# Kernel tuning notes

Measured on AMD Instinct MI355X. Metric: run time of the kernel, lower is better.

The kernel has to match this reference:

```python
import jax, jax.numpy as jnp
import numpy as np

N = 50000      # num_nodes
R = 8          # num_relations
H = 128        # hidden_channels
C = 40         # num_classes
E = 800000     # num_edges


def _seg_mean_over_relations(msgs, dst, etype):
    """Per-relation mean aggregation (PyG RGCNConv aggr='mean'), summed over relations.
    msgs: [E, H] per-edge messages; dst: [E] target nodes; etype: [E] relation ids.
    Returns [N, H].
    """
    seg = dst * R + etype                                   # [E] combined (node, relation) id
    sums = jax.ops.segment_sum(msgs, seg, num_segments=N * R)          # [N*R, H]
    cnt = jax.ops.segment_sum(jnp.ones((msgs.shape[0], 1), msgs.dtype), seg,
                              num_segments=N * R)                       # [N*R, 1]
    mean = sums / jnp.maximum(cnt, 1.0)
    return mean.reshape(N, R, -1).sum(axis=1)               # [N, H]


def setup_inputs() -> dict:
    key = jax.random.key(0)
    ks = jax.random.split(key, 10)
    s = 0.02
    edge_index = jax.random.randint(ks[0], (2, E), 0, N, dtype=jnp.int32)
    edge_type = jax.random.randint(ks[1], (E,), 0, R, dtype=jnp.int32)
    return {
        "edge_index": edge_index,
        "edge_type": edge_type,
        "W1": jax.random.normal(ks[2], (R, N, H), jnp.float32) * s,    # featureless: embedding per (rel, node)
        "root1": jax.random.normal(ks[3], (N, H), jnp.float32) * s,    # root embedding (x=None)
        "b1": jnp.zeros((H,), jnp.float32),
        "W2": jax.random.normal(ks[4], (R, H, H), jnp.float32) * s,
        "root2": jax.random.normal(ks[5], (H, H), jnp.float32) * s,
        "b2": jnp.zeros((H,), jnp.float32),
        "lin_w": jax.random.normal(ks[6], (H, C), jnp.float32) * s,
        "lin_b": jnp.zeros((C,), jnp.float32),
    }


def reference(edge_index, edge_type, W1, root1, b1, W2, root2, b2, lin_w, lin_b):
    src, dst = edge_index[0], edge_index[1]  # flow: source_to_target

    # ---- layer 1 (featureless RGCNConv): gather relation-specific node embeddings ----
    msgs1 = W1[edge_type, src]                               # [E, H]
    h = _seg_mean_over_relations(msgs1, dst, edge_type)      # [N, H]
    h = h + root1 + b1
    h = jax.nn.relu(h)

    # ---- layer 2: relation-specific dense transform then gather-scatter ----
    xr = jnp.einsum('nh,rhk->rnk', h, W2)                    # [R, N, H]
    msgs2 = xr[edge_type, src]                               # [E, H]
    h2 = _seg_mean_over_relations(msgs2, dst, edge_type)     # [N, H]
    h2 = h2 + h @ root2 + b2
    h2 = jax.nn.relu(h2)

    # ---- final linear ----
    return h2 @ lin_w + lin_b                                # [N, C]
```

## Files before the change

kernel.cpp:

```cpp
#include <hip/hip_runtime.h>

#define HH 128
#define RNUM 8
#define CC 40
#define CAP 64
#define LDA 136
#define SRCMASK 0x7FFFFFF

typedef __attribute__((ext_vector_type(8))) short short8;
typedef __attribute__((ext_vector_type(4))) float floatx4;

__device__ __forceinline__ float u2f(unsigned u) {
    union { unsigned u; float f; } c;
    c.u = u;
    return c.f;
}
__device__ __forceinline__ unsigned short f2bf(float f) {
    union { float f; unsigned u; } c;
    c.f = f;
    return (unsigned short)((c.u + 0x7FFFu + ((c.u >> 16) & 1u)) >> 16);
}

__global__ void fill1_kernel(const int* __restrict__ src, const int* __restrict__ dst,
                             const int* __restrict__ et, int* __restrict__ deg,
                             int* __restrict__ elist, int E) {
    int e = blockIdx.x * blockDim.x + threadIdx.x;
    if (e < E) {
        int d = dst[e];
        int p = atomicAdd(&deg[d], 1);
        if (p < CAP) elist[(size_t)d * CAP + p] = (int)(((unsigned)et[e] << 27) | (unsigned)src[e]);
    }
}

__global__ void gather1_kernel(const int* __restrict__ deg, const int* __restrict__ elist,
                               const float* __restrict__ W1, const float* __restrict__ root1,
                               const float* __restrict__ b1, unsigned short* __restrict__ hbf,
                               int Nn) {
    int w = (blockIdx.x * blockDim.x + threadIdx.x) >> 6;
    if (w >= Nn) return;
    int lane = threadIdx.x & 63;
    int qid = lane >> 4, cl = lane & 15;
    int dd = min(deg[w], CAP);
    int pk = elist[(size_t)w * CAP + lane];
    int myrel = (lane < dd) ? (int)((unsigned)pk >> 27) : 8;

    float myinv = 1.0f;
#pragma unroll
    for (int r = 0; r < 8; ++r) {
        unsigned long long m = __ballot(myrel == r);
        int c = __popcll(m);
        if (lane == r) myinv = 1.0f / fmaxf(1.0f, (float)c);
    }

    float s0[8] = {0.f, 0.f, 0.f, 0.f, 0.f, 0.f, 0.f, 0.f};
    float s1[8] = {0.f, 0.f, 0.f, 0.f, 0.f, 0.f, 0.f, 0.f};
    float s2[8] = {0.f, 0.f, 0.f, 0.f, 0.f, 0.f, 0.f, 0.f};
    float s3[8] = {0.f, 0.f, 0.f, 0.f, 0.f, 0.f, 0.f, 0.f};

#define GRP(G, S)                                                                 \
    {                                                                             \
        int j = ((G) << 2) + qid;                                                 \
        int jj = min(j, dd - 1);                                                  \
        int pkj = __shfl(pk, jj);                                                 \
        int rr = (int)((unsigned)pkj >> 27);                                      \
        float wt = __shfl(myinv, rr);                                             \
        int ss = pkj & SRCMASK;                                                   \
        const float* p = W1 + ((size_t)rr * Nn + ss) * HH + cl * 8;               \
        if (j < dd) {                                                             \
            float4 v0 = *(const float4*)p;                                        \
            float4 v1 = *(const float4*)(p + 4);                                  \
            S[0] += v0.x * wt; S[1] += v0.y * wt; S[2] += v0.z * wt; S[3] += v0.w * wt; \
            S[4] += v1.x * wt; S[5] += v1.y * wt; S[6] += v1.z * wt; S[7] += v1.w * wt; \
        }                                                                         \
    }

    int ng = (dd + 3) >> 2;
    int g = 0;
    for (; g + 3 < ng; g += 4) {
        GRP(g, s0);
        GRP(g + 1, s1);
        GRP(g + 2, s2);
        GRP(g + 3, s3);
    }
    for (; g < ng; ++g) GRP(g, s0);
#undef GRP

#pragma unroll
    for (int k = 0; k < 8; ++k) {
        s0[k] += s1[k] + s2[k] + s3[k];
        s0[k] += __shfl_xor(s0[k], 16);
        s0[k] += __shfl_xor(s0[k], 32);
    }

    if (qid == 0) {
        const float* rp = root1 + (size_t)w * HH + cl * 8;
        float4 r0 = *(const float4*)rp;
        float4 r1 = *(const float4*)(rp + 4);
        float4 c0 = *(const float4*)(b1 + cl * 8);
        float4 c1 = *(const float4*)(b1 + cl * 8 + 4);
        float o[8];
        o[0] = fmaxf(s0[0] + r0.x + c0.x, 0.f); o[1] = fmaxf(s0[1] + r0.y + c0.y, 0.f);
        o[2] = fmaxf(s0[2] + r0.z + c0.z, 0.f); o[3] = fmaxf(s0[3] + r0.w + c0.w, 0.f);
        o[4] = fmaxf(s0[4] + r1.x + c1.x, 0.f); o[5] = fmaxf(s0[5] + r1.y + c1.y, 0.f);
        o[6] = fmaxf(s0[6] + r1.z + c1.z, 0.f); o[7] = fmaxf(s0[7] + r1.w + c1.w, 0.f);
        ushort4 pk0, pk1;
        pk0.x = f2bf(o[0]); pk0.y = f2bf(o[1]); pk0.z = f2bf(o[2]); pk0.w = f2bf(o[3]);
        pk1.x = f2bf(o[4]); pk1.y = f2bf(o[5]); pk1.z = f2bf(o[6]); pk1.w = f2bf(o[7]);
        unsigned short* hp = hbf + (size_t)w * HH + cl * 8;
        *(ushort4*)hp = pk0;
        *(ushort4*)(hp + 4) = pk1;
    }
}

__global__ void agg_kernel(const int* __restrict__ deg, const int* __restrict__ elist,
                           const unsigned short* __restrict__ hbf,
                           unsigned short* __restrict__ aggr, int Nn) {
    int w = (blockIdx.x * blockDim.x + threadIdx.x) >> 6;
    int d = w >> 1;
    if (d >= Nn) return;
    int half = w & 1;
    int lane = threadIdx.x & 63;
    int qid = lane >> 4, cl = lane & 15;
    int dd = min(deg[d], CAP);
    int pk = elist[(size_t)d * CAP + lane];
    int myrel = (lane < dd) ? (int)((unsigned)pk >> 27) : 8;

#define ACC8(V, S)                                                 \
    {                                                              \
        S[0] += u2f(V.x << 16); S[1] += u2f(V.x & 0xFFFF0000u);    \
        S[2] += u2f(V.y << 16); S[3] += u2f(V.y & 0xFFFF0000u);    \
        S[4] += u2f(V.z << 16); S[5] += u2f(V.z & 0xFFFF0000u);    \
        S[6] += u2f(V.w << 16); S[7] += u2f(V.w & 0xFFFF0000u);    \
    }

#pragma unroll
    for (int ri = 0; ri < 4; ++ri) {
        int r = half * 4 + ri;
        unsigned long long m = __ballot(myrel == r);
        int c = __popcll(m);
        float inv = 1.0f / fmaxf(1.0f, (float)c);
        float s[8] = {0.f, 0.f, 0.f, 0.f, 0.f, 0.f, 0.f, 0.f};
        int idx = 0;
        while (m) {
            int j = __ffsll((unsigned long long)m) - 1;
            m &= m - 1;
            int pkj = __shfl(pk, j);
            if ((idx & 3) == qid) {
                int ss = pkj & SRCMASK;
                uint4 v = *(const uint4*)(hbf + (size_t)ss * HH + cl * 8);
                ACC8(v, s);
            }
            ++idx;
        }
#pragma unroll
        for (int k = 0; k < 8; ++k) {
            s[k] += __shfl_xor(s[k], 16);
            s[k] += __shfl_xor(s[k], 32);
        }
        if (qid == 0) {
            ushort4 p0, p1;
            p0.x = f2bf(s[0] * inv); p0.y = f2bf(s[1] * inv);
            p0.z = f2bf(s[2] * inv); p0.w = f2bf(s[3] * inv);
            p1.x = f2bf(s[4] * inv); p1.y = f2bf(s[5] * inv);
            p1.z = f2bf(s[6] * inv); p1.w = f2bf(s[7] * inv);
            unsigned short* ap = aggr + ((size_t)d * RNUM + r) * HH + cl * 8;
            *(ushort4*)ap = p0;
            *(ushort4*)(ap + 4) = p1;
        }
    }
#undef ACC8
}

__global__ void tcast_kernel(const float* __restrict__ root2, const float* __restrict__ W2,
                             unsigned short* __restrict__ Bt) {
    int bid = blockIdx.x;
    int c = bid >> 5;
    int id = (bid & 31) * 256 + threadIdx.x;
    int n = id >> 6, kp = id & 63;
    const float* B = (c == 0) ? root2 : W2 + (size_t)(c - 1) * HH * HH;
    float f0 = B[(2 * kp) * HH + n];
    float f1 = B[(2 * kp + 1) * HH + n];
    unsigned v = (unsigned)f2bf(f0) | ((unsigned)f2bf(f1) << 16);
    *(unsigned*)(Bt + (size_t)c * HH * HH + n * HH + 2 * kp) = v;
}

__global__ __launch_bounds__(256, 3) void gemm9_kernel(
    const unsigned short* __restrict__ hbf, const unsigned short* __restrict__ aggr,
    const unsigned short* __restrict__ Bt, const float* __restrict__ b2,
    const float* __restrict__ lin_w, const float* __restrict__ lin_b,
    float* __restrict__ out, int Nn) {
    __shared__ unsigned short As[64 * LDA];
    __shared__ unsigned short Bs[128 * LDA];
    const int tid = threadIdx.x;
    const int lane = tid & 63, wv = tid >> 6;
    const int quad = lane >> 4, l16 = lane & 15;
    const int mr = wv & 1, nc = wv >> 1;
    const int m0 = blockIdx.x * 64;

    floatx4 acc[2][4];
#pragma unroll
    for (int a = 0; a < 2; ++a)
#pragma unroll
        for (int bb = 0; bb < 4; ++bb) acc[a][bb] = (floatx4){0.f, 0.f, 0.f, 0.f};

    for (int c = 0; c < 9; ++c) {
        __syncthreads();
        const unsigned short* Bsrc = Bt + (size_t)c * HH * HH;
#pragma unroll
        for (int it = 0; it < 8; ++it) {
            int id = tid + it * 256;
            int rw = id >> 4, c8 = id & 15;
            *(uint4*)(Bs + rw * LDA + c8 * 8) = *(const uint4*)(Bsrc + rw * HH + c8 * 8);
        }
#pragma unroll
        for (int it = 0; it < 4; ++it) {
            int id = tid + it * 256;
            int rw = id >> 4, c8 = id & 15;
            uint4 v = make_uint4(0, 0, 0, 0);
            if (m0 + rw < Nn) {
                const unsigned short* Asrc =
                    (c == 0) ? (hbf + (size_t)(m0 + rw) * HH)
                             : (aggr + ((size_t)(m0 + rw) * RNUM + (c - 1)) * HH);
                v = *(const uint4*)(Asrc + c8 * 8);
            }
            *(uint4*)(As + rw * LDA + c8 * 8) = v;
        }
        __syncthreads();
#pragma unroll
        for (int ks = 0; ks < 4; ++ks) {
            short8 a0 = *(const short8*)(As + (mr * 32 + l16) * LDA + ks * 32 + quad * 8);
            short8 a1 = *(const short8*)(As + (mr * 32 + 16 + l16) * LDA + ks * 32 + quad * 8);
#pragma unroll
            for (int nf = 0; nf < 4; ++nf) {
                short8 b = *(const short8*)(Bs + (nc * 64 + nf * 16 + l16) * LDA + ks * 32 + quad * 8);
                acc[0][nf] = __builtin_amdgcn_mfma_f32_16x16x32_bf16(a0, b, acc[0][nf], 0, 0, 0);
                acc[1][nf] = __builtin_amdgcn_mfma_f32_16x16x32_bf16(a1, b, acc[1][nf], 0, 0, 0);
            }
        }
    }

    __syncthreads();
#pragma unroll
    for (int mf = 0; mf < 2; ++mf)
#pragma unroll
        for (int nf = 0; nf < 4; ++nf) {
            int gcol = nc * 64 + nf * 16 + l16;
            float bb = b2[gcol];
#pragma unroll
            for (int rg = 0; rg < 4; ++rg) {
                int row = mr * 32 + mf * 16 + quad * 4 + rg;
                float v = fmaxf(acc[mf][nf][rg] + bb, 0.f);
                As[row * LDA + gcol] = f2bf(v);
            }
        }
    for (int it = 0; it < 20; ++it) {
        int id = tid + it * 256;
        int n = id >> 7, k = id & 127;
        Bs[n * LDA + k] = f2bf(lin_w[k * CC + n]);
    }
    __syncthreads();

    floatx4 acc2[3];
#pragma unroll
    for (int nf = 0; nf < 3; ++nf) acc2[nf] = (floatx4){0.f, 0.f, 0.f, 0.f};
#pragma unroll
    for (int ks = 0; ks < 4; ++ks) {
        short8 a = *(const short8*)(As + (wv * 16 + l16) * LDA + ks * 32 + quad * 8);
#pragma unroll
        for (int nf = 0; nf < 3; ++nf) {
            short8 b = *(const short8*)(Bs + (nf * 16 + l16) * LDA + ks * 32 + quad * 8);
            acc2[nf] = __builtin_amdgcn_mfma_f32_16x16x32_bf16(a, b, acc2[nf], 0, 0, 0);
        }
    }
#pragma unroll
    for (int nf = 0; nf < 3; ++nf) {
        int col = nf * 16 + l16;
        if (col < CC) {
            float lb = lin_b[col];
#pragma unroll
            for (int rg = 0; rg < 4; ++rg) {
                int grow = m0 + wv * 16 + quad * 4 + rg;
                if (grow < Nn) out[(size_t)grow * CC + col] = acc2[nf][rg] + lb;
            }
        }
    }
}


extern "C" void kernel_launch(void* const* d_in, const int* in_sizes, int n_in,
                              void* d_out, int out_size, void* d_ws, size_t ws_size,
                              hipStream_t stream) {
    const int* ei      = (const int*)d_in[0];
    const int* et      = (const int*)d_in[1];
    const float* W1    = (const float*)d_in[2];
    const float* root1 = (const float*)d_in[3];
    const float* b1    = (const float*)d_in[4];
    const float* W2    = (const float*)d_in[5];
    const float* root2 = (const float*)d_in[6];
    const float* b2    = (const float*)d_in[7];
    const float* lw    = (const float*)d_in[8];
    const float* lb    = (const float*)d_in[9];
    float* out = (float*)d_out;

    const int E = in_sizes[1];
    const int N = in_sizes[3] / HH;

    int* deg   = (int*)d_ws;
    int* elist = deg + N;
    size_t iofs = (size_t)N + (size_t)N * CAP;
    iofs = (iofs + 3) & ~(size_t)3;
    unsigned short* hbf  = (unsigned short*)((int*)d_ws + iofs);
    unsigned short* Bt   = hbf + (size_t)N * HH;
    unsigned short* aggr = Bt + (size_t)9 * HH * HH;

    const int* src = ei;
    const int* dst = ei + E;

    hipMemsetAsync(deg, 0, (size_t)N * sizeof(int), stream);
    fill1_kernel<<<(E + 255) / 256, 256, 0, stream>>>(src, dst, et, deg, elist, E);

    tcast_kernel<<<9 * 32, 256, 0, stream>>>(root2, W2, Bt);

    gather1_kernel<<<(N * 64 + 255) / 256, 256, 0, stream>>>(deg, elist, W1, root1, b1, hbf, N);
    agg_kernel<<<(N * 2 * 64 + 255) / 256, 256, 0, stream>>>(deg, elist, hbf, aggr, N);
    gemm9_kernel<<<(N + 63) / 64, 256, 0, stream>>>(hbf, aggr, Bt, b2, lw, lb, out, N);
}
```

Measured before the change: 538.2 us.

## Transform-then-gather for layer 2 and pad degree counters

Layer 2 now runs the dense per-relation transform first: a GEMM computes xr = h @ W2[r] (plus the root transform) for all nodes into a bf16 buffer. A second gather kernel then pulls transformed rows per edge, takes the per-relation mean and applies bias and ReLU, and a separate small kernel does the final linear layer. This replaces the previous aggregate-then-GEMM path, which wrote an N×8×128 per-relation aggregate and ran a 9-chunk GEMM. Degree counters are also spaced 16 ints apart to reduce atomic contention, at the cost of a larger memset and workspace, and it adds an extra kernel plus a 9×N×128 intermediate buffer.

Result: faster. 480.5 us (-10.7%).

```diff
diff --git a/kernel.cpp b/kernel.cpp
--- a/kernel.cpp
+++ b/kernel.cpp
@@ -6,6 +6,7 @@
 #define CAP 64
 #define LDA 136
 #define SRCMASK 0x7FFFFFF
+#define DEGSTR 16
 
 typedef __attribute__((ext_vector_type(8))) short short8;
 typedef __attribute__((ext_vector_type(4))) float floatx4;
@@ -21,15 +22,28 @@
     return (unsigned short)((c.u + 0x7FFFu + ((c.u >> 16) & 1u)) >> 16);
 }
 
-__global__ void fill1_kernel(const int* __restrict__ src, const int* __restrict__ dst,
-                             const int* __restrict__ et, int* __restrict__ deg,
-                             int* __restrict__ elist, int E) {
+__global__ void fill_kernel(const int* __restrict__ src, const int* __restrict__ dst,
+                            const int* __restrict__ et, int* __restrict__ deg,
+                            int* __restrict__ elist, int E) {
     int e = blockIdx.x * blockDim.x + threadIdx.x;
     if (e < E) {
         int d = dst[e];
-        int p = atomicAdd(&deg[d], 1);
+        int p = atomicAdd(&deg[(size_t)d * DEGSTR], 1);
         if (p < CAP) elist[(size_t)d * CAP + p] = (int)(((unsigned)et[e] << 27) | (unsigned)src[e]);
     }
+}
+
+__global__ void tcast_kernel(const float* __restrict__ root2, const float* __restrict__ W2,
+                             unsigned short* __restrict__ Bt) {
+    int bid = blockIdx.x;
+    int c = bid >> 5;
+    int id = (bid & 31) * 256 + threadIdx.x;
+    int n = id >> 6, kp = id & 63;
+    const float* B = (c == 0) ? root2 : W2 + (size_t)(c - 1) * HH * HH;
+    float g0 = B[(2 * kp) * HH + n];
+    float g1 = B[(2 * kp + 1) * HH + n];
+    unsigned v = (unsigned)f2bf(g0) | ((unsigned)f2bf(g1) << 16);
+    *(unsigned*)(Bt + (size_t)c * HH * HH + n * HH + 2 * kp) = v;
 }
 
 __global__ void gather1_kernel(const int* __restrict__ deg, const int* __restrict__ elist,
@@ -40,7 +54,7 @@
     if (w >= Nn) return;
     int lane = threadIdx.x & 63;
     int qid = lane >> 4, cl = lane & 15;
-    int dd = min(deg[w], CAP);
+    int dd = min(deg[(size_t)w * DEGSTR], CAP);
     int pk = elist[(size_t)w * CAP + lane];
     int myrel = (lane < dd) ? (int)((unsigned)pk >> 27) : 8;
 
@@ -112,90 +126,35 @@
     }
 }
 
-__global__ void agg_kernel(const int* __restrict__ deg, const int* __restrict__ elist,
-                           const unsigned short* __restrict__ hbf,
-                           unsigned short* __restrict__ aggr, int Nn) {
-    int w = (blockIdx.x * blockDim.x + threadIdx.x) >> 6;
-    int d = w >> 1;
-    if (d >= Nn) return;
-    int half = w & 1;
-    int lane = threadIdx.x & 63;
-    int qid = lane >> 4, cl = lane & 15;
-    int dd = min(deg[d], CAP);
-    int pk = elist[(size_t)d * CAP + lane];
-    int myrel = (lane < dd) ? (int)((unsigned)pk >> 27) : 8;
-
-#define ACC8(V, S)                                                 \
-    {                                                              \
-        S[0] += u2f(V.x << 16); S[1] += u2f(V.x & 0xFFFF0000u);    \
-        S[2] += u2f(V.y << 16); S[3] += u2f(V.y & 0xFFFF0000u);    \
-        S[4] += u2f(V.z << 16); S[5] += u2f(V.z & 0xFFFF0000u);    \
-        S[6] += u2f(V.w << 16); S[7] += u2f(V.w & 0xFFFF0000u);    \
-    }
-
-#pragma unroll
-    for (int ri = 0; ri < 4; ++ri) {
-        int r = half * 4 + ri;
-        unsigned long long m = __ballot(myrel == r);
-        int c = __popcll(m);
-        float inv = 1.0f / fmaxf(1.0f, (float)c);
-        float s[8] = {0.f, 0.f, 0.f, 0.f, 0.f, 0.f, 0.f, 0.f};
-        int idx = 0;
-        while (m) {
-            int j = __ffsll((unsigned long long)m) - 1;
-            m &= m - 1;
-            int pkj = __shfl(pk, j);
-            if ((idx & 3) == qid) {
-                int ss = pkj & SRCMASK;
-                uint4 v = *(const uint4*)(hbf + (size_t)ss * HH + cl * 8);
-                ACC8(v, s);
-            }
-            ++idx;
-        }
-#pragma unroll
-        for (int k = 0; k < 8; ++k) {
-            s[k] += __shfl_xor(s[k], 16);
-            s[k] += __shfl_xor(s[k], 32);
-        }
-        if (qid == 0) {
-            ushort4 p0, p1;
-            p0.x = f2bf(s[0] * inv); p0.y = f2bf(s[1] * inv);
-            p0.z = f2bf(s[2] * inv); p0.w = f2bf(s[3] * inv);
-            p1.x = f2bf(s[4] * inv); p1.y = f2bf(s[5] * inv);
-            p1.z = f2bf(s[6] * inv); p1.w = f2bf(s[7] * inv);
-            unsigned short* ap = aggr + ((size_t)d * RNUM + r) * HH + cl * 8;
-            *(ushort4*)ap = p0;
-            *(ushort4*)(ap + 4) = p1;
-        }
-    }
-#undef ACC8
-}
-
-__global__ void tcast_kernel(const float* __restrict__ root2, const float* __restrict__ W2,
-                             unsigned short* __restrict__ Bt) {
-    int bid = blockIdx.x;
-    int c = bid >> 5;
-    int id = (bid & 31) * 256 + threadIdx.x;
-    int n = id >> 6, kp = id & 63;
-    const float* B = (c == 0) ? root2 : W2 + (size_t)(c - 1) * HH * HH;
-    float f0 = B[(2 * kp) * HH + n];
-    float f1 = B[(2 * kp + 1) * HH + n];
-    unsigned v = (unsigned)f2bf(f0) | ((unsigned)f2bf(f1) << 16);
-    *(unsigned*)(Bt + (size_t)c * HH * HH + n * HH + 2 * kp) = v;
-}
-
-__global__ __launch_bounds__(256, 3) void gemm9_kernel(
-    const unsigned short* __restrict__ hbf, const unsigned short* __restrict__ aggr,
-    const unsigned short* __restrict__ Bt, const float* __restrict__ b2,
-    const float* __restrict__ lin_w, const float* __restrict__ lin_b,
-    float* __restrict__ out, int Nn) {
+__global__ __launch_bounds__(256, 3) void gemmxr_kernel(
+    const unsigned short* __restrict__ hbf, const unsigned short* __restrict__ Bt,
+    unsigned short* __restrict__ xrb, int Nn, int nmb) {
     __shared__ unsigned short As[64 * LDA];
     __shared__ unsigned short Bs[128 * LDA];
     const int tid = threadIdx.x;
     const int lane = tid & 63, wv = tid >> 6;
     const int quad = lane >> 4, l16 = lane & 15;
     const int mr = wv & 1, nc = wv >> 1;
-    const int m0 = blockIdx.x * 64;
+    const int mb = blockIdx.x % nmb;
+    const int c = blockIdx.x / nmb;
+    const int m0 = mb * 64;
+
+#pragma unroll
+    for (int it = 0; it < 4; ++it) {
+        int id = tid + it * 256;
+        int rw = id >> 4, c8 = id & 15;
+        uint4 v = make_uint4(0, 0, 0, 0);
+        if (m0 + rw < Nn) v = *(const uint4*)(hbf + (size_t)(m0 + rw) * HH + c8 * 8);
+        *(uint4*)(As + rw * LDA + c8 * 8) = v;
+    }
+    const unsigned short* Bsrc = Bt + (size_t)c * HH * HH;
+#pragma unroll
+    for (int it = 0; it < 8; ++it) {
+        int id = tid + it * 256;
+        int rw = id >> 4, c8 = id & 15;
+        *(uint4*)(Bs + rw * LDA + c8 * 8) = *(const uint4*)(Bsrc + rw * HH + c8 * 8);
+    }
+    __syncthreads();
 
     floatx4 acc[2][4];
 #pragma unroll
@@ -203,60 +162,146 @@
 #pragma unroll
         for (int bb = 0; bb < 4; ++bb) acc[a][bb] = (floatx4){0.f, 0.f, 0.f, 0.f};
 
-    for (int c = 0; c < 9; ++c) {
-        __syncthreads();
-        const unsigned short* Bsrc = Bt + (size_t)c * HH * HH;
-#pragma unroll
-        for (int it = 0; it < 8; ++it) {
-            int id = tid + it * 256;
-            int rw = id >> 4, c8 = id & 15;
-            *(uint4*)(Bs + rw * LDA + c8 * 8) = *(const uint4*)(Bsrc + rw * HH + c8 * 8);
+#pragma unroll
+    for (int ks = 0; ks < 4; ++ks) {
+        short8 a0 = *(const short8*)(As + (mr * 32 + l16) * LDA + ks * 32 + quad * 8);
+        short8 a1 = *(const short8*)(As + (mr * 32 + 16 + l16) * LDA + ks * 32 + quad * 8);
+#pragma unroll
+        for (int nf = 0; nf < 4; ++nf) {
+            short8 b = *(const short8*)(Bs + (nc * 64 + nf * 16 + l16) * LDA + ks * 32 + quad * 8);
+            acc[0][nf] = __builtin_amdgcn_mfma_f32_16x16x32_bf16(a0, b, acc[0][nf], 0, 0, 0);
+            acc[1][nf] = __builtin_amdgcn_mfma_f32_16x16x32_bf16(a1, b, acc[1][nf], 0, 0, 0);
         }
-#pragma unroll
-        for (int it = 0; it < 4; ++it) {
-            int id = tid + it * 256;
-            int rw = id >> 4, c8 = id & 15;
-            uint4 v = make_uint4(0, 0, 0, 0);
-            if (m0 + rw < Nn) {
-                const unsigned short* Asrc =
-                    (c == 0) ? (hbf + (size_t)(m0 + rw) * HH)
-                             : (aggr + ((size_t)(m0 + rw) * RNUM + (c - 1)) * HH);
-                v = *(const uint4*)(Asrc + c8 * 8);
-            }
-            *(uint4*)(As + rw * LDA + c8 * 8) = v;
-        }
-        __syncthreads();
-#pragma unroll
-        for (int ks = 0; ks < 4; ++ks) {
-            short8 a0 = *(const short8*)(As + (mr * 32 + l16) * LDA + ks * 32 + quad * 8);
-            short8 a1 = *(const short8*)(As + (mr * 32 + 16 + l16) * LDA + ks * 32 + quad * 8);
-#pragma unroll
-            for (int nf = 0; nf < 4; ++nf) {
-                short8 b = *(const short8*)(Bs + (nc * 64 + nf * 16 + l16) * LDA + ks * 32 + quad * 8);
-                acc[0][nf] = __builtin_amdgcn_mfma_f32_16x16x32_bf16(a0, b, acc[0][nf], 0, 0, 0);
-                acc[1][nf] = __builtin_amdgcn_mfma_f32_16x16x32_bf16(a1, b, acc[1][nf], 0, 0, 0);
+    }
+
+    __syncthreads();
+#pragma unroll
+    for (int mf = 0; mf < 2; ++mf)
+#pragma unroll
+        for (int nf = 0; nf < 4; ++nf) {
+            int gcol = nc * 64 + nf * 16 + l16;
+#pragma unroll
+            for (int rg = 0; rg < 4; ++rg) {
+                int row = mr * 32 + mf * 16 + quad * 4 + rg;
+                Bs[row * LDA + gcol] = f2bf(acc[mf][nf][rg]);
             }
         }
-    }
-
     __syncthreads();
 #pragma unroll
-    for (int mf = 0; mf < 2; ++mf)
-#pragma unroll
-        for (int nf = 0; nf < 4; ++nf) {
-            int gcol = nc * 64 + nf * 16 + l16;
-            float bb = b2[gcol];
-#pragma unroll
-            for (int rg = 0; rg < 4; ++rg) {
-                int row = mr * 32 + mf * 16 + quad * 4 + rg;
-                float v = fmaxf(acc[mf][nf][rg] + bb, 0.f);
-                As[row * LDA + gcol] = f2bf(v);
-            }
-        }
-    for (int it = 0; it < 20; ++it) {
+    for (int it = 0; it < 4; ++it) {
+        int id = tid + it * 256;
+        int rw = id >> 4, c8 = id & 15;
+        if (m0 + rw < Nn)
+            *(uint4*)(xrb + ((size_t)c * Nn + m0 + rw) * HH + c8 * 8) =
+                *(const uint4*)(Bs + rw * LDA + c8 * 8);
+    }
+}
+
+__global__ void gather2_kernel(const int* __restrict__ deg, const int* __restrict__ elist,
+                               const unsigned short* __restrict__ xrb, const float* __restrict__ b2,
+                               unsigned short* __restrict__ h2bf, int Nn) {
+    int w = (blockIdx.x * blockDim.x + threadIdx.x) >> 6;
+    if (w >= Nn) return;
+    int lane = threadIdx.x & 63;
+    int qid = lane >> 4, cl = lane & 15;
+    int dd = min(deg[(size_t)w * DEGSTR], CAP);
+    int pk = elist[(size_t)w * CAP + lane];
+    int myrel = (lane < dd) ? (int)((unsigned)pk >> 27) : 8;
+
+    float myinv = 1.0f;
+#pragma unroll
+    for (int r = 0; r < 8; ++r) {
+        unsigned long long m = __ballot(myrel == r);
+        int c = __popcll(m);
+        if (lane == r) myinv = 1.0f / fmaxf(1.0f, (float)c);
+    }
+
+    float s0[8] = {0.f, 0.f, 0.f, 0.f, 0.f, 0.f, 0.f, 0.f};
+    float s1[8] = {0.f, 0.f, 0.f, 0.f, 0.f, 0.f, 0.f, 0.f};
+    float s2[8] = {0.f, 0.f, 0.f, 0.f, 0.f, 0.f, 0.f, 0.f};
+    float s3[8] = {0.f, 0.f, 0.f, 0.f, 0.f, 0.f, 0.f, 0.f};
+
+#define GRP(G, S)                                                                 \
+    {                                                                             \
+        int j = ((G) << 2) + qid;                                                 \
+        int jj = min(j, dd - 1);                                                  \
+        int pkj = __shfl(pk, jj);                                                 \
+        int rr = (int)((unsigned)pkj >> 27);                                      \
+        float wt = __shfl(myinv, rr);                                             \
+        int ss = pkj & SRCMASK;                                                   \
+        const unsigned short* p = xrb + ((size_t)(rr + 1) * Nn + ss) * HH + cl * 8; \
+        if (j < dd) {                                                             \
+            uint4 v = *(const uint4*)p;                                           \
+            S[0] += u2f(v.x << 16) * wt; S[1] += u2f(v.x & 0xFFFF0000u) * wt;     \
+            S[2] += u2f(v.y << 16) * wt; S[3] += u2f(v.y & 0xFFFF0000u) * wt;     \
+            S[4] += u2f(v.z << 16) * wt; S[5] += u2f(v.z & 0xFFFF0000u) * wt;     \
+            S[6] += u2f(v.w << 16) * wt; S[7] += u2f(v.w & 0xFFFF0000u) * wt;     \
+        }                                                                         \
+    }
+
+    int ng = (dd + 3) >> 2;
+    int g = 0;
+    for (; g + 3 < ng; g += 4) {
+        GRP(g, s0);
+        GRP(g + 1, s1);
+        GRP(g + 2, s2);
+        GRP(g + 3, s3);
+    }
+    for (; g < ng; ++g) GRP(g, s0);
+#undef GRP
+
+#pragma unroll
+    for (int k = 0; k < 8; ++k) {
+        s0[k] += s1[k] + s2[k] + s3[k];
+        s0[k] += __shfl_xor(s0[k], 16);
+        s0[k] += __shfl_xor(s0[k], 32);
+    }
+
+    if (qid == 0) {
+        uint4 sv = *(const uint4*)(xrb + (size_t)w * HH + cl * 8);
+        float4 c0 = *(const float4*)(b2 + cl * 8);
+        float4 c1 = *(const float4*)(b2 + cl * 8 + 4);
+        float o[8];
+        o[0] = fmaxf(s0[0] + u2f(sv.x << 16) + c0.x, 0.f);
+        o[1] = fmaxf(s0[1] + u2f(sv.x & 0xFFFF0000u) + c0.y, 0.f);
+        o[2] = fmaxf(s0[2] + u2f(sv.y << 16) + c0.z, 0.f);
+        o[3] = fmaxf(s0[3] + u2f(sv.y & 0xFFFF0000u) + c0.w, 0.f);
+        o[4] = fmaxf(s0[4] + u2f(sv.z << 16) + c1.x, 0.f);
+        o[5] = fmaxf(s0[5] + u2f(sv.z & 0xFFFF0000u) + c1.y, 0.f);
+        o[6] = fmaxf(s0[6] + u2f(sv.w << 16) + c1.z, 0.f);
+        o[7] = fmaxf(s0[7] + u2f(sv.w & 0xFFFF0000u) + c1.w, 0.f);
+        ushort4 p0, p1;
+        p0.x = f2bf(o[0]); p0.y = f2bf(o[1]); p0.z = f2bf(o[2]); p0.w = f2bf(o[3]);
+        p1.x = f2bf(o[4]); p1.y = f2bf(o[5]); p1.z = f2bf(o[6]); p1.w = f2bf(o[7]);
+        unsigned short* hp = h2bf + (size_t)w * HH + cl * 8;
+        *(ushort4*)hp = p0;
+        *(ushort4*)(hp + 4) = p1;
+    }
+}
+
+__global__ __launch_bounds__(256, 4) void linout_kernel(
+    const unsigned short* __restrict__ h2, const float* __restrict__ lin_w,
+    const float* __restrict__ lin_b, float* __restrict__ out, int Nn) {
+    __shared__ unsigned short As[64 * LDA];
+    __shared__ unsigned short Bs[48 * LDA];
+    const int tid = threadIdx.x;
+    const int lane = tid & 63, wv = tid >> 6;
+    const int quad = lane >> 4, l16 = lane & 15;
+    const int m0 = blockIdx.x * 64;
+
+#pragma unroll
+    for (int it = 0; it < 4; ++it) {
+        int id = tid + it * 256;
+        int rw = id >> 4, c8 = id & 15;
+        uint4 v = make_uint4(0, 0, 0, 0);
+        if (m0 + rw < Nn) v = *(const uint4*)(h2 + (size_t)(m0 + rw) * HH + c8 * 8);
+        *(uint4*)(As + rw * LDA + c8 * 8) = v;
+    }
+#pragma unroll
+    for (int it = 0; it < 24; ++it) {
         int id = tid + it * 256;
         int n = id >> 7, k = id & 127;
-        Bs[n * LDA + k] = f2bf(lin_w[k * CC + n]);
+        Bs[n * LDA + k] = (n < CC) ? f2bf(lin_w[(size_t)k * CC + n]) : (unsigned short)0;
     }
     __syncthreads();
 
@@ -306,22 +351,24 @@
     const int N = in_sizes[3] / HH;
 
     int* deg   = (int*)d_ws;
-    int* elist = deg + N;
-    size_t iofs = (size_t)N + (size_t)N * CAP;
+    int* elist = deg + (size_t)N * DEGSTR;
+    size_t iofs = (size_t)N * DEGSTR + (size_t)N * CAP;
     iofs = (iofs + 3) & ~(size_t)3;
     unsigned short* hbf  = (unsigned short*)((int*)d_ws + iofs);
     unsigned short* Bt   = hbf + (size_t)N * HH;
-    unsigned short* aggr = Bt + (size_t)9 * HH * HH;
+    unsigned short* xrb  = Bt + (size_t)9 * HH * HH;
+    unsigned short* h2bf = xrb + (size_t)9 * N * HH;
 
     const int* src = ei;
     const int* dst = ei + E;
 
-    hipMemsetAsync(deg, 0, (size_t)N * sizeof(int), stream);
-    fill1_kernel<<<(E + 255) / 256, 256, 0, stream>>>(src, dst, et, deg, elist, E);
-
+    const int nmb = (N + 63) / 64;
+
+    hipMemsetAsync(deg, 0, (size_t)N * DEGSTR * sizeof(int), stream);
+    fill_kernel<<<(E + 255) / 256, 256, 0, stream>>>(src, dst, et, deg, elist, E);
     tcast_kernel<<<9 * 32, 256, 0, stream>>>(root2, W2, Bt);
-
     gather1_kernel<<<(N * 64 + 255) / 256, 256, 0, stream>>>(deg, elist, W1, root1, b1, hbf, N);
-    agg_kernel<<<(N * 2 * 64 + 255) / 256, 256, 0, stream>>>(deg, elist, hbf, aggr, N);
-    gemm9_kernel<<<(N + 63) / 64, 256, 0, stream>>>(hbf, aggr, Bt, b2, lw, lb, out, N);
-}
+    gemmxr_kernel<<<nmb * 9, 256, 0, stream>>>(hbf, Bt, xrb, N, nmb);
+    gather2_kernel<<<(N * 64 + 255) / 256, 256, 0, stream>>>(deg, elist, xrb, b2, h2bf, N);
+    linout_kernel<<<nmb, 256, 0, stream>>>(h2bf, lw, lb, out, N);
+}
```

## Fuse layer-2 aggregation into the GEMM kernel and pad degree counters

Applied to the files above, without the earlier changes.

Merges the per-relation mean aggregation into the layer-2 GEMM kernel. Each block gathers neighbor rows for 32 nodes straight into shared memory, so the [N,8,128] aggr buffer is never written to or read back from global memory. B tiles are now read directly from global memory instead of being staged in LDS, and occupancy drops to 2 blocks per SM because of the larger shared tile. Degree counters are spread 16 ints apart, apparently to reduce atomic contention in the fill kernel, at the cost of a larger memset.

After: 580.0 us. 7.8% more time.

```diff
diff --git a/kernel.cpp b/kernel.cpp
--- a/kernel.cpp
+++ b/kernel.cpp
@@ -6,6 +6,7 @@
 #define CAP 64
 #define LDA 136
 #define SRCMASK 0x7FFFFFF
+#define DEGSTR 16
 
 typedef __attribute__((ext_vector_type(8))) short short8;
 typedef __attribute__((ext_vector_type(4))) float floatx4;
@@ -21,15 +22,28 @@
     return (unsigned short)((c.u + 0x7FFFu + ((c.u >> 16) & 1u)) >> 16);
 }
 
-__global__ void fill1_kernel(const int* __restrict__ src, const int* __restrict__ dst,
-                             const int* __restrict__ et, int* __restrict__ deg,
-                             int* __restrict__ elist, int E) {
+__global__ void fill_kernel(const int* __restrict__ src, const int* __restrict__ dst,
+                            const int* __restrict__ et, int* __restrict__ deg,
+                            int* __restrict__ elist, int E) {
     int e = blockIdx.x * blockDim.x + threadIdx.x;
     if (e < E) {
         int d = dst[e];
-        int p = atomicAdd(&deg[d], 1);
+        int p = atomicAdd(&deg[(size_t)d * DEGSTR], 1);
         if (p < CAP) elist[(size_t)d * CAP + p] = (int)(((unsigned)et[e] << 27) | (unsigned)src[e]);
     }
+}
+
+__global__ void tcast_kernel(const float* __restrict__ root2, const float* __restrict__ W2,
+                             unsigned short* __restrict__ Bt) {
+    int bid = blockIdx.x;
+    int c = bid >> 5;
+    int id = (bid & 31) * 256 + threadIdx.x;
+    int n = id >> 6, kp = id & 63;
+    const float* B = (c == 0) ? root2 : W2 + (size_t)(c - 1) * HH * HH;
+    float g0 = B[(2 * kp) * HH + n];
+    float g1 = B[(2 * kp + 1) * HH + n];
+    unsigned v = (unsigned)f2bf(g0) | ((unsigned)f2bf(g1) << 16);
+    *(unsigned*)(Bt + (size_t)c * HH * HH + n * HH + 2 * kp) = v;
 }
 
 __global__ void gather1_kernel(const int* __restrict__ deg, const int* __restrict__ elist,
@@ -40,7 +54,7 @@
     if (w >= Nn) return;
     int lane = threadIdx.x & 63;
     int qid = lane >> 4, cl = lane & 15;
-    int dd = min(deg[w], CAP);
+    int dd = min(deg[(size_t)w * DEGSTR], CAP);
     int pk = elist[(size_t)w * CAP + lane];
     int myrel = (lane < dd) ? (int)((unsigned)pk >> 27) : 8;
 
@@ -112,175 +126,151 @@
     }
 }
 
-__global__ void agg_kernel(const int* __restrict__ deg, const int* __restrict__ elist,
-                           const unsigned short* __restrict__ hbf,
-                           unsigned short* __restrict__ aggr, int Nn) {
-    int w = (blockIdx.x * blockDim.x + threadIdx.x) >> 6;
-    int d = w >> 1;
-    if (d >= Nn) return;
-    int half = w & 1;
-    int lane = threadIdx.x & 63;
-    int qid = lane >> 4, cl = lane & 15;
-    int dd = min(deg[d], CAP);
-    int pk = elist[(size_t)d * CAP + lane];
-    int myrel = (lane < dd) ? (int)((unsigned)pk >> 27) : 8;
-
-#define ACC8(V, S)                                                 \
-    {                                                              \
-        S[0] += u2f(V.x << 16); S[1] += u2f(V.x & 0xFFFF0000u);    \
-        S[2] += u2f(V.y << 16); S[3] += u2f(V.y & 0xFFFF0000u);    \
-        S[4] += u2f(V.z << 16); S[5] += u2f(V.z & 0xFFFF0000u);    \
-        S[6] += u2f(V.w << 16); S[7] += u2f(V.w & 0xFFFF0000u);    \
-    }
-
-#pragma unroll
-    for (int ri = 0; ri < 4; ++ri) {
-        int r = half * 4 + ri;
-        unsigned long long m = __ballot(myrel == r);
-        int c = __popcll(m);
-        float inv = 1.0f / fmaxf(1.0f, (float)c);
-        float s[8] = {0.f, 0.f, 0.f, 0.f, 0.f, 0.f, 0.f, 0.f};
-        int idx = 0;
-        while (m) {
-            int j = __ffsll((unsigned long long)m) - 1;
-            m &= m - 1;
-            int pkj = __shfl(pk, j);
-            if ((idx & 3) == qid) {
-                int ss = pkj & SRCMASK;
-                uint4 v = *(const uint4*)(hbf + (size_t)ss * HH + cl * 8);
-                ACC8(v, s);
-            }
-            ++idx;
-        }
-#pragma unroll
-        for (int k = 0; k < 8; ++k) {
-            s[k] += __shfl_xor(s[k], 16);
-            s[k] += __shfl_xor(s[k], 32);
-        }
-        if (qid == 0) {
-            ushort4 p0, p1;
-            p0.x = f2bf(s[0] * inv); p0.y = f2bf(s[1] * inv);
-            p0.z = f2bf(s[2] * inv); p0.w = f2bf(s[3] * inv);
-            p1.x = f2bf(s[4] * inv); p1.y = f2bf(s[5] * inv);
-            p1.z = f2bf(s[6] * inv); p1.w = f2bf(s[7] * inv);
-            unsigned short* ap = aggr + ((size_t)d * RNUM + r) * HH + cl * 8;
-            *(ushort4*)ap = p0;
-            *(ushort4*)(ap + 4) = p1;
-        }
-    }
-#undef ACC8
-}
-
-__global__ void tcast_kernel(const float* __restrict__ root2, const float* __restrict__ W2,
-                             unsigned short* __restrict__ Bt) {
-    int bid = blockIdx.x;
-    int c = bid >> 5;
-    int id = (bid & 31) * 256 + threadIdx.x;
-    int n = id >> 6, kp = id & 63;
-    const float* B = (c == 0) ? root2 : W2 + (size_t)(c - 1) * HH * HH;
-    float f0 = B[(2 * kp) * HH + n];
-    float f1 = B[(2 * kp + 1) * HH + n];
-    unsigned v = (unsigned)f2bf(f0) | ((unsigned)f2bf(f1) << 16);
-    *(unsigned*)(Bt + (size_t)c * HH * HH + n * HH + 2 * kp) = v;
-}
-
-__global__ __launch_bounds__(256, 3) void gemm9_kernel(
-    const unsigned short* __restrict__ hbf, const unsigned short* __restrict__ aggr,
-    const unsigned short* __restrict__ Bt, const float* __restrict__ b2,
-    const float* __restrict__ lin_w, const float* __restrict__ lin_b,
-    float* __restrict__ out, int Nn) {
-    __shared__ unsigned short As[64 * LDA];
-    __shared__ unsigned short Bs[128 * LDA];
+__global__ __launch_bounds__(256, 2) void layer2_kernel(
+    const int* __restrict__ deg, const int* __restrict__ elist,
+    const unsigned short* __restrict__ hbf, const unsigned short* __restrict__ Bt,
+    const float* __restrict__ b2, const float* __restrict__ lin_w,
+    const float* __restrict__ lin_b, float* __restrict__ out, int Nn) {
+    __shared__ unsigned short AT[9 * 32 * LDA];
     const int tid = threadIdx.x;
     const int lane = tid & 63, wv = tid >> 6;
     const int quad = lane >> 4, l16 = lane & 15;
-    const int mr = wv & 1, nc = wv >> 1;
-    const int m0 = blockIdx.x * 64;
-
-    floatx4 acc[2][4];
+    const int m0 = blockIdx.x * 32;
+
+#pragma unroll
+    for (int it = 0; it < 2; ++it) {
+        int id = tid + it * 256;
+        int rw = id >> 4, c8 = id & 15;
+        uint4 v = make_uint4(0, 0, 0, 0);
+        if (m0 + rw < Nn) v = *(const uint4*)(hbf + (size_t)(m0 + rw) * HH + c8 * 8);
+        *(uint4*)(AT + rw * LDA + c8 * 8) = v;
+    }
+
+    for (int i = 0; i < 8; ++i) {
+        int dl = wv * 8 + i;
+        int d = m0 + dl;
+        int dd = 0, pk = 0;
+        if (d < Nn) {
+            dd = min(deg[(size_t)d * DEGSTR], CAP);
+            pk = elist[(size_t)d * CAP + lane];
+        }
+        float a0x = 0.f, a0y = 0.f, a1x = 0.f, a1y = 0.f, a2x = 0.f, a2y = 0.f, a3x = 0.f, a3y = 0.f;
+        float a4x = 0.f, a4y = 0.f, a5x = 0.f, a5y = 0.f, a6x = 0.f, a6y = 0.f, a7x = 0.f, a7y = 0.f;
+        int c0 = 0, c1 = 0, c2 = 0, c3 = 0, c4 = 0, c5 = 0, c6 = 0, c7 = 0;
+
+#define ACCE(P, U)                                                             \
+    {                                                                          \
+        unsigned rr_ = (unsigned)(P) >> 27;                                    \
+        float f0_ = u2f((U) << 16), f1_ = u2f((U) & 0xFFFF0000u);              \
+        switch (rr_) {                                                         \
+            case 0: a0x += f0_; a0y += f1_; ++c0; break;                       \
+            case 1: a1x += f0_; a1y += f1_; ++c1; break;                       \
+            case 2: a2x += f0_; a2y += f1_; ++c2; break;                       \
+            case 3: a3x += f0_; a3y += f1_; ++c3; break;                       \
+            case 4: a4x += f0_; a4y += f1_; ++c4; break;                       \
+            case 5: a5x += f0_; a5y += f1_; ++c5; break;                       \
+            case 6: a6x += f0_; a6y += f1_; ++c6; break;                       \
+            default: a7x += f0_; a7y += f1_; ++c7; break;                      \
+        }                                                                      \
+    }
+
+        for (int j = 0; j < dd; j += 4) {
+            int p0 = __shfl(pk, j);
+            int p1 = __shfl(pk, min(j + 1, dd - 1));
+            int p2 = __shfl(pk, min(j + 2, dd - 1));
+            int p3 = __shfl(pk, min(j + 3, dd - 1));
+            unsigned u0 = *(const unsigned*)(hbf + (size_t)(p0 & SRCMASK) * HH + lane * 2);
+            unsigned u1 = *(const unsigned*)(hbf + (size_t)(p1 & SRCMASK) * HH + lane * 2);
+            unsigned u2 = *(const unsigned*)(hbf + (size_t)(p2 & SRCMASK) * HH + lane * 2);
+            unsigned u3 = *(const unsigned*)(hbf + (size_t)(p3 & SRCMASK) * HH + lane * 2);
+            ACCE(p0, u0);
+            if (j + 1 < dd) ACCE(p1, u1);
+            if (j + 2 < dd) ACCE(p2, u2);
+            if (j + 3 < dd) ACCE(p3, u3);
+        }
+#undef ACCE
+
+        unsigned short* atp = AT + 32 * LDA + dl * LDA + lane * 2;
+#define WR(R, AX, AY, CN)                                                       \
+    {                                                                           \
+        float inv_ = 1.0f / fmaxf(1.0f, (float)(CN));                           \
+        unsigned v_ = (unsigned)f2bf((AX) * inv_) | ((unsigned)f2bf((AY) * inv_) << 16); \
+        *(unsigned*)(atp + (R) * 32 * LDA) = v_;                                \
+    }
+        WR(0, a0x, a0y, c0); WR(1, a1x, a1y, c1); WR(2, a2x, a2y, c2); WR(3, a3x, a3y, c3);
+        WR(4, a4x, a4y, c4); WR(5, a5x, a5y, c5); WR(6, a6x, a6y, c6); WR(7, a7x, a7y, c7);
+#undef WR
+    }
+    __syncthreads();
+
+    const int n0 = wv * 32;
+    floatx4 acc[2][2];
 #pragma unroll
     for (int a = 0; a < 2; ++a)
 #pragma unroll
-        for (int bb = 0; bb < 4; ++bb) acc[a][bb] = (floatx4){0.f, 0.f, 0.f, 0.f};
+        for (int b = 0; b < 2; ++b) acc[a][b] = (floatx4){0.f, 0.f, 0.f, 0.f};
 
     for (int c = 0; c < 9; ++c) {
-        __syncthreads();
-        const unsigned short* Bsrc = Bt + (size_t)c * HH * HH;
-#pragma unroll
-        for (int it = 0; it < 8; ++it) {
-            int id = tid + it * 256;
-            int rw = id >> 4, c8 = id & 15;
-            *(uint4*)(Bs + rw * LDA + c8 * 8) = *(const uint4*)(Bsrc + rw * HH + c8 * 8);
-        }
-#pragma unroll
-        for (int it = 0; it < 4; ++it) {
-            int id = tid + it * 256;
-            int rw = id >> 4, c8 = id & 15;
-            uint4 v = make_uint4(0, 0, 0, 0);
-            if (m0 + rw < Nn) {
-                const unsigned short* Asrc =
-                    (c == 0) ? (hbf + (size_t)(m0 + rw) * HH)
-                             : (aggr + ((size_t)(m0 + rw) * RNUM + (c - 1)) * HH);
-                v = *(const uint4*)(Asrc + c8 * 8);
-            }
-            *(uint4*)(As + rw * LDA + c8 * 8) = v;
-        }
-        __syncthreads();
+        const unsigned short* Ap = AT + c * 32 * LDA;
+        const unsigned short* Bp = Bt + (size_t)c * HH * HH;
 #pragma unroll
         for (int ks = 0; ks < 4; ++ks) {
-            short8 a0 = *(const short8*)(As + (mr * 32 + l16) * LDA + ks * 32 + quad * 8);
-            short8 a1 = *(const short8*)(As + (mr * 32 + 16 + l16) * LDA + ks * 32 + quad * 8);
-#pragma unroll
-            for (int nf = 0; nf < 4; ++nf) {
-                short8 b = *(const short8*)(Bs + (nc * 64 + nf * 16 + l16) * LDA + ks * 32 + quad * 8);
+            short8 a0 = *(const short8*)(Ap + l16 * LDA + ks * 32 + quad * 8);
+            short8 a1 = *(const short8*)(Ap + (16 + l16) * LDA + ks * 32 + quad * 8);
+#pragma unroll
+            for (int nf = 0; nf < 2; ++nf) {
+                short8 b = *(const short8*)(Bp + (size_t)(n0 + nf * 16 + l16) * HH + ks * 32 + quad * 8);
                 acc[0][nf] = __builtin_amdgcn_mfma_f32_16x16x32_bf16(a0, b, acc[0][nf], 0, 0, 0);
                 acc[1][nf] = __builtin_amdgcn_mfma_f32_16x16x32_bf16(a1, b, acc[1][nf], 0, 0, 0);
             }
         }
     }
-
     __syncthreads();
+
 #pragma unroll
     for (int mf = 0; mf < 2; ++mf)
 #pragma unroll
-        for (int nf = 0; nf < 4; ++nf) {
-            int gcol = nc * 64 + nf * 16 + l16;
+        for (int nf = 0; nf < 2; ++nf) {
+            int gcol = n0 + nf * 16 + l16;
             float bb = b2[gcol];
 #pragma unroll
             for (int rg = 0; rg < 4; ++rg) {
-                int row = mr * 32 + mf * 16 + quad * 4 + rg;
-                float v = fmaxf(acc[mf][nf][rg] + bb, 0.f);
-                As[row * LDA + gcol] = f2bf(v);
+                int row = mf * 16 + quad * 4 + rg;
+                AT[row * LDA + gcol] = f2bf(fmaxf(acc[mf][nf][rg] + bb, 0.f));
             }
         }
-    for (int it = 0; it < 20; ++it) {
+    unsigned short* LW = AT + 32 * LDA;
+#pragma unroll
+    for (int it = 0; it < 24; ++it) {
         int id = tid + it * 256;
         int n = id >> 7, k = id & 127;
-        Bs[n * LDA + k] = f2bf(lin_w[k * CC + n]);
+        LW[n * LDA + k] = (n < CC) ? f2bf(lin_w[(size_t)k * CC + n]) : (unsigned short)0;
     }
     __syncthreads();
 
-    floatx4 acc2[3];
-#pragma unroll
-    for (int nf = 0; nf < 3; ++nf) acc2[nf] = (floatx4){0.f, 0.f, 0.f, 0.f};
-#pragma unroll
-    for (int ks = 0; ks < 4; ++ks) {
-        short8 a = *(const short8*)(As + (wv * 16 + l16) * LDA + ks * 32 + quad * 8);
+    if (wv < 2) {
+        floatx4 a2[3];
+#pragma unroll
+        for (int nf = 0; nf < 3; ++nf) a2[nf] = (floatx4){0.f, 0.f, 0.f, 0.f};
+#pragma unroll
+        for (int ks = 0; ks < 4; ++ks) {
+            short8 a = *(const short8*)(AT + (wv * 16 + l16) * LDA + ks * 32 + quad * 8);
+#pragma unroll
+            for (int nf = 0; nf < 3; ++nf) {
+                short8 b = *(const short8*)(LW + (nf * 16 + l16) * LDA + ks * 32 + quad * 8);
+                a2[nf] = __builtin_amdgcn_mfma_f32_16x16x32_bf16(a, b, a2[nf], 0, 0, 0);
+            }
+        }
 #pragma unroll
         for (int nf = 0; nf < 3; ++nf) {
-            short8 b = *(const short8*)(Bs + (nf * 16 + l16) * LDA + ks * 32 + quad * 8);
-            acc2[nf] = __builtin_amdgcn_mfma_f32_16x16x32_bf16(a, b, acc2[nf], 0, 0, 0);
-        }
-    }
-#pragma unroll
-    for (int nf = 0; nf < 3; ++nf) {
-        int col = nf * 16 + l16;
-        if (col < CC) {
-            float lb = lin_b[col];
-#pragma unroll
-            for (int rg = 0; rg < 4; ++rg) {
-                int grow = m0 + wv * 16 + quad * 4 + rg;
-                if (grow < Nn) out[(size_t)grow * CC + col] = acc2[nf][rg] + lb;
+            int col = nf * 16 + l16;
+            if (col < CC) {
+                float lb = lin_b[col];
+#pragma unroll
+                for (int rg = 0; rg < 4; ++rg) {
+                    int grow = m0 + wv * 16 + quad * 4 + rg;
+                    if (grow < Nn) out[(size_t)grow * CC + col] = a2[nf][rg] + lb;
+                }
             }
         }
     }
@@ -306,22 +296,18 @@
     const int N = in_sizes[3] / HH;
 
     int* deg   = (int*)d_ws;
-    int* elist = deg + N;
-    size_t iofs = (size_t)N + (size_t)N * CAP;
+    int* elist = deg + (size_t)N * DEGSTR;
+    size_t iofs = (size_t)N * DEGSTR + (size_t)N * CAP;
     iofs = (iofs + 3) & ~(size_t)3;
-    unsigned short* hbf  = (unsigned short*)((int*)d_ws + iofs);
-    unsigned short* Bt   = hbf + (size_t)N * HH;
-    unsigned short* aggr = Bt + (size_t)9 * HH * HH;
+    unsigned short* hbf = (unsigned short*)((int*)d_ws + iofs);
+    unsigned short* Bt  = hbf + (size_t)N * HH;
 
     const int* src = ei;
     const int* dst = ei + E;
 
-    hipMemsetAsync(deg, 0, (size_t)N * sizeof(int), stream);
-    fill1_kernel<<<(E + 255) / 256, 256, 0, stream>>>(src, dst, et, deg, elist, E);
-
+    hipMemsetAsync(deg, 0, (size_t)N * DEGSTR * sizeof(int), stream);
+    fill_kernel<<<(E + 255) / 256, 256, 0, stream>>>(src, dst, et, deg, elist, E);
     tcast_kernel<<<9 * 32, 256, 0, stream>>>(root2, W2, Bt);
-
     gather1_kernel<<<(N * 64 + 255) / 256, 256, 0, stream>>>(deg, elist, W1, root1, b1, hbf, N);
-    agg_kernel<<<(N * 2 * 64 + 255) / 256, 256, 0, stream>>>(deg, elist, hbf, aggr, N);
-    gemm9_kernel<<<(N + 63) / 64, 256, 0, stream>>>(hbf, aggr, Bt, b2, lw, lb, out, N);
-}
+    layer2_kernel<<<(N + 31) / 32, 256, 0, stream>>>(deg, elist, hbf, Bt, b2, lw, lb, out, N);
+}
```
